# Optimization experiments

Measured on AMD Instinct MI355X. Metric: run time of the kernel, lower is better.

## Reference

```python
import jax, jax.numpy as jnp
import numpy as np

NUM_HEADS = 32
NUM_KV_HEADS = 8
HEAD_DIM = 128
HIDDEN = 4096
THETA = 10000.0


def apply_rotary_emb(x, theta=THETA):
    # x: (B, S, H, D). Torch code converts to complex with real = first half
    # of last dim, imag = second half (rotate-half convention).
    B, S, H, D = x.shape
    half = D // 2
    freqs = 1.0 / theta ** (jnp.arange(0, D, 2, dtype=jnp.float32) / D)  # (half,)
    t = jnp.arange(S, dtype=jnp.float32)
    ang = jnp.outer(t, freqs)  # (S, half)
    cos = jnp.cos(ang)[None, :, None, :]  # (1,S,1,half)
    sin = jnp.sin(ang)[None, :, None, :]
    x1, x2 = x[..., :half], x[..., half:]
    out = jnp.concatenate([x1 * cos - x2 * sin, x1 * sin + x2 * cos], axis=-1)
    return out.astype(x.dtype)


def setup_inputs() -> dict:
    key = jax.random.key(0)
    k1, k2, k3 = jax.random.split(key, 3)
    B, S = 1, 2048
    qkv_out = (NUM_HEADS + 2 * NUM_KV_HEADS) * HEAD_DIM  # 6144
    hidden_states = jax.random.normal(k1, (B, S, HIDDEN), dtype=jnp.float32)
    w_qkv = jax.random.normal(k2, (qkv_out, HIDDEN), dtype=jnp.float32) * 0.02
    w_o = jax.random.normal(k3, (HIDDEN, NUM_HEADS * HEAD_DIM), dtype=jnp.float32) * 0.02
    return {"hidden_states": hidden_states, "w_qkv": w_qkv, "w_o": w_o}


def reference(hidden_states, w_qkv, w_o):
    B, S, _ = hidden_states.shape
    q_size = NUM_HEADS * HEAD_DIM
    kv_size = NUM_KV_HEADS * HEAD_DIM
    n_rep = NUM_HEADS // NUM_KV_HEADS

    qkv = hidden_states @ w_qkv.T  # (B,S,6144)
    xq = qkv[..., :q_size].reshape(B, S, NUM_HEADS, HEAD_DIM)
    xk = qkv[..., q_size:q_size + kv_size].reshape(B, S, NUM_KV_HEADS, HEAD_DIM)
    xv = qkv[..., q_size + kv_size:].reshape(B, S, NUM_KV_HEADS, HEAD_DIM)

    xq = apply_rotary_emb(xq)
    xk = apply_rotary_emb(xk)

    # repeat_interleave KV heads to match query heads
    xk = jnp.repeat(xk, n_rep, axis=2)
    xv = jnp.repeat(xv, n_rep, axis=2)

    q = xq.transpose(0, 2, 1, 3)  # (B,H,S,D)
    k = xk.transpose(0, 2, 1, 3)
    v = xv.transpose(0, 2, 1, 3)

    scale = 1.0 / np.sqrt(HEAD_DIM).astype(np.float32)
    scores = jnp.einsum('bhqd,bhkd->bhqk', q, k) * scale
    causal = jnp.tril(jnp.ones((S, S), dtype=bool))
    scores = jnp.where(causal[None, None], scores, jnp.float32(-jnp.inf))
    attn = jax.nn.softmax(scores, axis=-1)  # dropout=0 (eval)
    out = jnp.einsum('bhqk,bhkd->bhqd', attn, v)
    out = out.transpose(0, 2, 1, 3).reshape(B, S, NUM_HEADS * HEAD_DIM)
    return out @ w_o.T
```

## Files before the change

kernel.cpp:

```cpp
#include <hip/hip_runtime.h>
#include <cstdint>

#define S_LEN 2048
#define HID   4096
#define NHQ   32
#define NKV   8
#define HD    128
#define QKV_N 6144

typedef float  f32x4 __attribute__((ext_vector_type(4)));
typedef short  s16x8 __attribute__((ext_vector_type(8)));
typedef unsigned short ushort_t;

typedef __attribute__((address_space(3))) void       lds_void;
typedef const __attribute__((address_space(1))) void gbl_void;

__device__ __forceinline__ void gload_lds16(const void* g, void* l) {
  __builtin_amdgcn_global_load_lds((gbl_void*)g, (lds_void*)l, 16, 0, 0);
}

__device__ __forceinline__ short f2bf_bits(float f) {
  union { __bf16 b; short s; } u;
  u.b = (__bf16)f;
  return u.s;
}
__device__ __forceinline__ float bf2f(unsigned short u) {
  union { unsigned int i; float f; } x;
  x.i = ((unsigned int)u) << 16;
  return x.f;
}

__device__ __forceinline__ void cvt8(const float* src, ushort_t* dst, int j) {
  const f32x4* s = (const f32x4*)src;
  f32x4 a = s[j * 2], b = s[j * 2 + 1];
  s16x8 r;
  r[0] = f2bf_bits(a[0]); r[1] = f2bf_bits(a[1]); r[2] = f2bf_bits(a[2]); r[3] = f2bf_bits(a[3]);
  r[4] = f2bf_bits(b[0]); r[5] = f2bf_bits(b[1]); r[6] = f2bf_bits(b[2]); r[7] = f2bf_bits(b[3]);
  *((s16x8*)dst + j) = r;
}

__global__ __launch_bounds__(256)
void cvt_hw(const float* __restrict__ h, const float* __restrict__ wq,
            ushort_t* __restrict__ hb, ushort_t* __restrict__ wqb) {
  int i = blockIdx.x * 256 + threadIdx.x;
  if (i < 1048576) cvt8(h, hb, i);
  else             cvt8(wq, wqb, i - 1048576);
}

template <int N> __device__ __forceinline__ void wait_vm() {
  if constexpr (N == 6)      asm volatile("s_waitcnt vmcnt(6)" ::: "memory");
  else if constexpr (N == 4) asm volatile("s_waitcnt vmcnt(4)" ::: "memory");
  else                       asm volatile("s_waitcnt vmcnt(0)" ::: "memory");
}

template <bool OUTF32>
__global__ __launch_bounds__(512, 2)
void gemm8p(const ushort_t* __restrict__ Ag, const ushort_t* __restrict__ Bg,
            void* __restrict__ Cp, int M, int N, int K) {
  __shared__ __align__(16) ushort_t As[2][2][256 * 32];
  __shared__ __align__(16) ushort_t Bs[2][2][256 * 32];

  const int t = threadIdx.x;
  const int w = t >> 6, l = t & 63;
  const int n16 = l & 15, quad = l >> 4;
  const int wm = w >> 2, wn = w & 3;
  const int sw16 = (quad ^ (n16 & 3)) * 16;
  const int m0 = blockIdx.x * 256, n0 = blockIdx.y * 256;

  const int srow = t >> 2;
  const int schunk = (t & 3) ^ (srow & 3);
  const ushort_t* Abase = Ag + (size_t)(m0 + srow) * K + schunk * 8;
  const ushort_t* Bbase = Bg + (size_t)(n0 + srow) * K + schunk * 8;
  char* AsB = (char*)&As[0][0][0];
  char* BsB = (char*)&Bs[0][0][0];
  const size_t hstep = (size_t)128 * K;

  auto stageA = [&](int b, int h, int tile) {
    const ushort_t* g = Abase + (size_t)h * hstep + tile * 64;
    gload_lds16(g,      AsB + b * 32768 + h * 8192 + t * 16);
    gload_lds16(g + 32, AsB + b * 32768 + 16384 + h * 8192 + t * 16);
  };
  auto stageB = [&](int b, int h, int tile) {
    const ushort_t* g = Bbase + (size_t)h * hstep + tile * 64;
    gload_lds16(g,      BsB + b * 32768 + h * 8192 + t * 16);
    gload_lds16(g + 32, BsB + b * 32768 + 16384 + h * 8192 + t * 16);
  };

  const int aRowBase = wm * 64 + n16;
  const int bRowBase = wn * 32 + n16;
  const char* AsR = (const char*)AsB;
  const char* BsR = (const char*)BsB;

  f32x4 acc[8][4] = {};
  s16x8 af[4][2];

#define PHASE(b, qm, qn, STAGE, WZ) do {                                            \
    if ((qn) == 0) {                                                                \
      _Pragma("unroll")                                                             \
      for (int mf = 0; mf < 4; mf++)                                                \
        _Pragma("unroll")                                                           \
        for (int ks = 0; ks < 2; ks++)                                              \
          af[mf][ks] = *(const s16x8*)(AsR + (b) * 32768 + ks * 16384 +             \
                        ((qm) * 128 + mf * 16 + aRowBase) * 64 + sw16);             \
    }                                                                               \
    s16x8 bf[2][2];                                                                 \
    _Pragma("unroll")                                                               \
    for (int nf = 0; nf < 2; nf++)                                                  \
      _Pragma("unroll")                                                             \
      for (int ks = 0; ks < 2; ks++)                                                \
        bf[nf][ks] = *(const s16x8*)(BsR + (b) * 32768 + ks * 16384 +               \
                      ((qn) * 128 + nf * 16 + bRowBase) * 64 + sw16);               \
    __builtin_amdgcn_s_setprio(1);                                                  \
    _Pragma("unroll")                                                               \
    for (int ks = 0; ks < 2; ks++)                                                  \
      _Pragma("unroll")                                                             \
      for (int mf = 0; mf < 4; mf++)                                                \
        _Pragma("unroll")                                                           \
        for (int nf = 0; nf < 2; nf++)                                              \
          acc[(qm) * 4 + mf][(qn) * 2 + nf] = __builtin_amdgcn_mfma_f32_16x16x32_bf16( \
              af[mf][ks], bf[nf][ks], acc[(qm) * 4 + mf][(qn) * 2 + nf], 0, 0, 0);  \
    __builtin_amdgcn_s_setprio(0);                                                  \
    STAGE;                                                                          \
    if (WZ) wait_vm<0>(); else wait_vm<6>();                                        \
    asm volatile("" ::: "memory");                                                  \
    __builtin_amdgcn_s_barrier();                                                   \
    asm volatile("" ::: "memory");                                                  \
  } while (0)

  const int NT = K >> 6;
  const int NI = NT >> 1;

  stageA(0, 0, 0); stageA(0, 1, 0); stageB(0, 0, 0); stageB(0, 1, 0);
  stageA(1, 0, 1); stageB(1, 0, 1);
  wait_vm<4>();
  asm volatile("" ::: "memory");
  __builtin_amdgcn_s_barrier();
  asm volatile("" ::: "memory");

  for (int i = 0; i < NI - 1; i++) {
    const int tp1 = 2 * i + 1, tp2 = 2 * i + 2, tp3 = 2 * i + 3;
    PHASE(0, 0, 0, stageA(1, 1, tp1), 0);
    PHASE(0, 0, 1, stageB(1, 1, tp1), 0);
    PHASE(0, 1, 0, stageA(0, 0, tp2), 0);
    PHASE(0, 1, 1, stageB(0, 0, tp2), 0);
    PHASE(1, 0, 0, stageA(0, 1, tp2), 0);
    PHASE(1, 0, 1, stageB(0, 1, tp2), 0);
    PHASE(1, 1, 0, stageA(1, 0, tp3), 0);
    PHASE(1, 1, 1, stageB(1, 0, tp3), 0);
  }
  PHASE(0, 0, 0, stageA(1, 1, NT - 1), 0);
  PHASE(0, 0, 1, stageB(1, 1, NT - 1), 0);
  PHASE(0, 1, 0, ((void)0), 0);
  PHASE(0, 1, 1, ((void)0), 1);
  PHASE(1, 0, 0, ((void)0), 1);
  PHASE(1, 0, 1, ((void)0), 1);
  PHASE(1, 1, 0, ((void)0), 1);
  PHASE(1, 1, 1, ((void)0), 1);
#undef PHASE

#pragma unroll
  for (int a = 0; a < 8; a++)
#pragma unroll
    for (int bq = 0; bq < 4; bq++)
#pragma unroll
      for (int r = 0; r < 4; r++) {
        int row = m0 + (a >> 2) * 128 + wm * 64 + (a & 3) * 16 + quad * 4 + r;
        int col = n0 + (bq >> 1) * 128 + wn * 32 + (bq & 1) * 16 + n16;
        float v = acc[a][bq][r];
        if constexpr (OUTF32) ((float*)Cp)[(size_t)row * N + col] = v;
        else ((ushort_t*)Cp)[(size_t)row * N + col] = (ushort_t)f2bf_bits(v);
      }
}

__global__ __launch_bounds__(256)
void rope_vt_cvtwo(const ushort_t* __restrict__ qkv, ushort_t* __restrict__ Q,
                   ushort_t* __restrict__ Kc, ushort_t* __restrict__ Vt,
                   const float* __restrict__ wo, ushort_t* __restrict__ wob) {
  __shared__ __align__(16) ushort_t tile[64][72];
  const int b = blockIdx.x;
  const int t = threadIdx.x;
  if (b < 2048) {
    const int s = b;
    const float LN1E4_64 = 0.14391156831212787f;
    for (int item = t; item < (NHQ + NKV) * 64; item += 256) {
      int head = item >> 6, i = item & 63;
      float f = expf(-(float)i * LN1E4_64);
      float ang = (float)s * f;
      float sn, cs;
      sincosf(ang, &sn, &cs);
      if (head < NHQ) {
        const ushort_t* src = qkv + (size_t)s * QKV_N + head * HD;
        float x1 = bf2f(src[i]), x2 = bf2f(src[64 + i]);
        const float sc = 0.08838834764831845f;
        ushort_t* dst = Q + ((size_t)head * S_LEN + s) * HD;
        dst[i]      = (ushort_t)f2bf_bits((x1 * cs - x2 * sn) * sc);
        dst[64 + i] = (ushort_t)f2bf_bits((x1 * sn + x2 * cs) * sc);
      } else {
        int kv = head - NHQ;
        const ushort_t* src = qkv + (size_t)s * QKV_N + 4096 + kv * HD;
        float x1 = bf2f(src[i]), x2 = bf2f(src[64 + i]);
        ushort_t* dst = Kc + ((size_t)kv * S_LEN + s) * HD;
        dst[i]      = (ushort_t)f2bf_bits(x1 * cs - x2 * sn);
        dst[64 + i] = (ushort_t)f2bf_bits(x1 * sn + x2 * cs);
      }
    }
  } else if (b < 2560) {
    const int bb = b - 2048;
    const int s0 = (bb & 31) * 64;
    const int by = bb >> 5;
    const int kv = by >> 1;
    const int d0 = (by & 1) * 64;
    {
      int r = t >> 2, c = (t & 3) * 16;
      const ushort_t* src = qkv + (size_t)(s0 + r) * QKV_N + 5120 + kv * HD + d0 + c;
      *(s16x8*)&tile[r][c]     = *(const s16x8*)src;
      *(s16x8*)&tile[r][c + 8] = *(const s16x8*)(src + 8);
    }
    __syncthreads();
    {
      int d = t >> 2, sseg = (t & 3) * 16;
      ushort_t* dst = Vt + ((size_t)kv * HD + d0 + d) * S_LEN + s0 + sseg;
      s16x8 o1, o2;
#pragma unroll
      for (int i = 0; i < 8; i++) { o1[i] = tile[sseg + i][d]; o2[i] = tile[sseg + 8 + i][d]; }
      *(s16x8*)dst = o1;
      *(s16x8*)(dst + 8) = o2;
    }
  } else {
    int j = (b - 2560) * 256 + t;
    cvt8(wo, wob, j);
  }
}

__global__ __launch_bounds__(256)
void attn_kernel(const ushort_t* __restrict__ Q, const ushort_t* __restrict__ Kc,
                 const ushort_t* __restrict__ Vt, ushort_t* __restrict__ Out) {
  __shared__ __align__(16) ushort_t Ks[2][64 * 128];
  __shared__ __align__(16) ushort_t Vs[2][128 * 64];
  __shared__ __align__(16) ushort_t Pl[4][16 * 72];
  const int bx = blockIdx.x;
  const int h = blockIdx.y;
  const int t = threadIdx.x, w = t >> 6, l = t & 63;
  const int n16 = l & 15, quad = l >> 4;
  const int kv = h >> 2;
  const ushort_t* Qh = Q  + (size_t)h  * S_LEN * HD;
  const ushort_t* Kh = Kc + (size_t)kv * S_LEN * HD;
  const ushort_t* Vh = Vt + (size_t)kv * HD * S_LEN;

  const int qtA = bx, qtB = 31 - bx;
  const int q0A = qtA * 64 + w * 16, q0B = qtB * 64 + w * 16;
  const int tripsA = qtA + 1;
  const int TOTAL = 33;

  s16x8 qfA[4], qfB[4];
#pragma unroll
  for (int ks = 0; ks < 4; ks++) {
    qfA[ks] = *(const s16x8*)(Qh + (size_t)(q0A + n16) * HD + ks * 32 + quad * 8);
    qfB[ks] = *(const s16x8*)(Qh + (size_t)(q0B + n16) * HD + ks * 32 + quad * 8);
  }

  s16x8 ones;
  {
    short v = (n16 == 0) ? (short)0x3F80 : (short)0;
#pragma unroll
    for (int j = 0; j < 8; j++) ones[j] = v;
  }

  f32x4 o[9] = {};
  float mrun[4] = {-1e30f, -1e30f, -1e30f, -1e30f};

  ushort_t* P = Pl[w];

  auto stage = [&](int k0, int buf) {
#pragma unroll
    for (int c = 0; c < 4; c++) {
      int idx = (c * 4 + w) * 64 + l;
      int row = idx >> 4, sc = idx & 15;
      int dseg = sc ^ (row & 15);
      gload_lds16(Kh + (size_t)(k0 + row) * HD + dseg * 8,
                  (char*)&Ks[buf][0] + (c * 4 + w) * 1024);
    }
#pragma unroll
    for (int c = 0; c < 4; c++) {
      int idx = (c * 4 + w) * 64 + l;
      int row = idx >> 3, sc = idx & 7;
      int ks2 = sc ^ (row & 7);
      gload_lds16(Vh + (size_t)row * S_LEN + k0 + ks2 * 8,
                  (char*)&Vs[buf][0] + (c * 4 + w) * 1024);
    }
  };

  stage(0, 0);

  for (int i = 0; i < TOTAL; i++) {
    const bool isA = (i < tripsA);
    const int kt = isA ? i : i - tripsA;
    const int q0 = isA ? q0A : q0B;
    const int k0 = kt * 64;
    const int buf = i & 1;

    __syncthreads();

    if (i + 1 < TOTAL) {
      const bool nA = (i + 1 < tripsA);
      const int nkt = nA ? (i + 1) : (i + 1 - tripsA);
      stage(nkt * 64, buf ^ 1);
    }

    const ushort_t* KsB = &Ks[buf][0];
    const ushort_t* VsB = &Vs[buf][0];

    f32x4 sacc[4] = {};
#pragma unroll
    for (int ks = 0; ks < 4; ks++) {
      s16x8 qf = isA ? qfA[ks] : qfB[ks];
#pragma unroll
      for (int nt = 0; nt < 4; nt++) {
        int row = nt * 16 + n16;
        s16x8 kf = *(const s16x8*)(KsB + row * 128 + ((ks * 4 + quad) ^ (row & 15)) * 8);
        sacc[nt] = __builtin_amdgcn_mfma_f32_16x16x32_bf16(qf, kf, sacc[nt], 0, 0, 0);
      }
    }

    if (k0 + 63 > q0) {
#pragma unroll
      for (int nt = 0; nt < 4; nt++)
#pragma unroll
        for (int r = 0; r < 4; r++) {
          int qrow = q0 + quad * 4 + r;
          int key  = k0 + nt * 16 + n16;
          if (key > qrow) sacc[nt][r] = -1e30f;
        }
    }

#pragma unroll
    for (int r = 0; r < 4; r++) {
      float tmx = fmaxf(fmaxf(sacc[0][r], sacc[1][r]), fmaxf(sacc[2][r], sacc[3][r]));
#pragma unroll
      for (int d = 1; d < 16; d <<= 1) tmx = fmaxf(tmx, __shfl_xor(tmx, d));
      float nm = fmaxf(mrun[r], tmx);
      float alpha = __expf(mrun[r] - nm);
      mrun[r] = nm;
#pragma unroll
      for (int nt = 0; nt < 4; nt++) sacc[nt][r] = __expf(sacc[nt][r] - nm);
#pragma unroll
      for (int nt2 = 0; nt2 < 9; nt2++) o[nt2][r] *= alpha;
    }

#pragma unroll
    for (int nt = 0; nt < 4; nt++)
#pragma unroll
      for (int r = 0; r < 4; r++)
        P[(quad * 4 + r) * 72 + nt * 16 + n16] = (ushort_t)f2bf_bits(sacc[nt][r]);
    asm volatile("s_waitcnt lgkmcnt(0)" ::: "memory");
    s16x8 pa[2];
#pragma unroll
    for (int kseg = 0; kseg < 2; kseg++)
      pa[kseg] = *(const s16x8*)(P + n16 * 72 + kseg * 32 + quad * 8);

#pragma unroll
    for (int kseg = 0; kseg < 2; kseg++) {
#pragma unroll
      for (int ntd = 0; ntd < 8; ntd++) {
        int row = ntd * 16 + n16;
        s16x8 vf = *(const s16x8*)(VsB + row * 64 + ((kseg * 4 + quad) ^ (row & 7)) * 8);
        o[ntd] = __builtin_amdgcn_mfma_f32_16x16x32_bf16(pa[kseg], vf, o[ntd], 0, 0, 0);
      }
      o[8] = __builtin_amdgcn_mfma_f32_16x16x32_bf16(pa[kseg], ones, o[8], 0, 0, 0);
    }

    if (i == tripsA - 1) {
#pragma unroll
      for (int r = 0; r < 4; r++) {
        float lsum = __shfl(o[8][r], l & 48);
        float inv = 1.0f / lsum;
        int qrow = q0A + quad * 4 + r;
#pragma unroll
        for (int ntd = 0; ntd < 8; ntd++)
          Out[(size_t)qrow * HID + h * HD + ntd * 16 + n16] = (ushort_t)f2bf_bits(o[ntd][r] * inv);
      }
#pragma unroll
      for (int nt2 = 0; nt2 < 9; nt2++) o[nt2] = (f32x4){0.f, 0.f, 0.f, 0.f};
#pragma unroll
      for (int r = 0; r < 4; r++) mrun[r] = -1e30f;
    }
  }

#pragma unroll
  for (int r = 0; r < 4; r++) {
    float lsum = __shfl(o[8][r], l & 48);
    float inv = 1.0f / lsum;
    int qrow = q0B + quad * 4 + r;
#pragma unroll
    for (int ntd = 0; ntd < 8; ntd++)
      Out[(size_t)qrow * HID + h * HD + ntd * 16 + n16] = (ushort_t)f2bf_bits(o[ntd][r] * inv);
  }
}

extern "C" void kernel_launch(void* const* d_in, const int* in_sizes, int n_in,
                              void* d_out, int out_size, void* d_ws, size_t ws_size,
                              hipStream_t stream) {
  const float* hidden = (const float*)d_in[0];
  const float* w_qkv  = (const float*)d_in[1];
  const float* w_o    = (const float*)d_in[2];
  float* out = (float*)d_out;
  char* ws = (char*)d_ws;

  ushort_t* hidden_bf = (ushort_t*)ws;
  ushort_t* Qb        = (ushort_t*)ws;
  ushort_t* wqkv_bf   = (ushort_t*)(ws + 16777216);
  ushort_t* wo_bf     = (ushort_t*)(ws + 16777216);
  ushort_t* qkv       = (ushort_t*)(ws + 67108864);
  ushort_t* attn_out  = (ushort_t*)(ws + 67108864);
  ushort_t* Kb        = (ushort_t*)(ws + 92274688);
  ushort_t* Vtb       = (ushort_t*)(ws + 96468992);

  cvt_hw<<<dim3(16384), 256, 0, stream>>>(hidden, w_qkv, hidden_bf, wqkv_bf);
  gemm8p<false><<<dim3(8, 24), 512, 0, stream>>>(hidden_bf, wqkv_bf, (void*)qkv, 2048, 6144, 4096);
  rope_vt_cvtwo<<<dim3(10752), 256, 0, stream>>>(qkv, Qb, Kb, Vtb, w_o, wo_bf);
  attn_kernel<<<dim3(16, 32), 256, 0, stream>>>(Qb, Kb, Vtb, attn_out);
  gemm8p<true><<<dim3(8, 16), 512, 0, stream>>>(attn_out, wo_bf, (void*)out, 2048, 4096, 4096);
}
```

Measured before the change: 560.2 us.

## Restructure GEMM main loop into serpentine phases with B-fragment register reuse

Reworks the 256x256 bf16 GEMM inner loop so each phase issues its LDS reads and next global-to-LDS stage before a barrier and then runs the MFMAs. The quadrant order now snakes (00,01,11,10) so A or B fragments are reused across consecutive phases, using two B fragment register sets. This cuts LDS read traffic. Vmem waits happen only every fourth phase instead of every phase, and the prologue prefetch order changes to match. The cost is more registers, and the barrier and lgkm wait placement adds risk of stalls or races if the staging order is off.

```diff
diff --git a/kernel.cpp b/kernel.cpp
--- a/kernel.cpp
+++ b/kernel.cpp
@@ -88,75 +88,82 @@
 
   const int aRowBase = wm * 64 + n16;
   const int bRowBase = wn * 32 + n16;
-  const char* AsR = (const char*)AsB;
-  const char* BsR = (const char*)BsB;
 
   f32x4 acc[8][4] = {};
-  s16x8 af[4][2];
-
-#define PHASE(b, qm, qn, STAGE, WZ) do {                                            \
-    if ((qn) == 0) {                                                                \
-      _Pragma("unroll")                                                             \
-      for (int mf = 0; mf < 4; mf++)                                                \
-        _Pragma("unroll")                                                           \
-        for (int ks = 0; ks < 2; ks++)                                              \
-          af[mf][ks] = *(const s16x8*)(AsR + (b) * 32768 + ks * 16384 +             \
-                        ((qm) * 128 + mf * 16 + aRowBase) * 64 + sw16);             \
-    }                                                                               \
-    s16x8 bf[2][2];                                                                 \
-    _Pragma("unroll")                                                               \
-    for (int nf = 0; nf < 2; nf++)                                                  \
-      _Pragma("unroll")                                                             \
-      for (int ks = 0; ks < 2; ks++)                                                \
-        bf[nf][ks] = *(const s16x8*)(BsR + (b) * 32768 + ks * 16384 +               \
-                      ((qn) * 128 + nf * 16 + bRowBase) * 64 + sw16);               \
-    __builtin_amdgcn_s_setprio(1);                                                  \
-    _Pragma("unroll")                                                               \
-    for (int ks = 0; ks < 2; ks++)                                                  \
-      _Pragma("unroll")                                                             \
-      for (int mf = 0; mf < 4; mf++)                                                \
-        _Pragma("unroll")                                                           \
-        for (int nf = 0; nf < 2; nf++)                                              \
-          acc[(qm) * 4 + mf][(qn) * 2 + nf] = __builtin_amdgcn_mfma_f32_16x16x32_bf16( \
-              af[mf][ks], bf[nf][ks], acc[(qm) * 4 + mf][(qn) * 2 + nf], 0, 0, 0);  \
-    __builtin_amdgcn_s_setprio(0);                                                  \
-    STAGE;                                                                          \
-    if (WZ) wait_vm<0>(); else wait_vm<6>();                                        \
-    asm volatile("" ::: "memory");                                                  \
-    __builtin_amdgcn_s_barrier();                                                   \
-    asm volatile("" ::: "memory");                                                  \
+  s16x8 af[4][2], bf0[2][2], bf1[2][2];
+
+#define RD_A(b, qm) do {                                                        \
+    _Pragma("unroll")                                                           \
+    for (int mf = 0; mf < 4; mf++)                                              \
+      _Pragma("unroll")                                                         \
+      for (int ks = 0; ks < 2; ks++)                                            \
+        af[mf][ks] = *(const s16x8*)(AsB + (b) * 32768 + ks * 16384 +           \
+                      ((qm) * 128 + mf * 16 + aRowBase) * 64 + sw16);           \
+  } while (0)
+
+#define RD_B(b, qn, dst) do {                                                   \
+    _Pragma("unroll")                                                           \
+    for (int nf = 0; nf < 2; nf++)                                              \
+      _Pragma("unroll")                                                         \
+      for (int ks = 0; ks < 2; ks++)                                            \
+        dst[nf][ks] = *(const s16x8*)(BsB + (b) * 32768 + ks * 16384 +          \
+                      ((qn) * 128 + nf * 16 + bRowBase) * 64 + sw16);           \
+  } while (0)
+
+#define PHASE(RDS, STG, qm, qn, BFX, VMW) do {                                  \
+    RDS;                                                                        \
+    STG;                                                                        \
+    __builtin_amdgcn_s_barrier();                                               \
+    asm volatile("s_waitcnt lgkmcnt(0)" ::: "memory");                          \
+    __builtin_amdgcn_sched_barrier(0);                                          \
+    __builtin_amdgcn_s_setprio(1);                                              \
+    _Pragma("unroll")                                                           \
+    for (int ks = 0; ks < 2; ks++)                                              \
+      _Pragma("unroll")                                                         \
+      for (int mf = 0; mf < 4; mf++)                                            \
+        _Pragma("unroll")                                                       \
+        for (int nf = 0; nf < 2; nf++)                                          \
+          acc[(qm) * 4 + mf][(qn) * 2 + nf] =                                   \
+            __builtin_amdgcn_mfma_f32_16x16x32_bf16(af[mf][ks], BFX[nf][ks],    \
+                acc[(qm) * 4 + mf][(qn) * 2 + nf], 0, 0, 0);                    \
+    __builtin_amdgcn_s_setprio(0);                                              \
+    VMW;                                                                        \
+    __builtin_amdgcn_s_barrier();                                               \
+    asm volatile("" ::: "memory");                                              \
   } while (0)
 
   const int NT = K >> 6;
   const int NI = NT >> 1;
 
-  stageA(0, 0, 0); stageA(0, 1, 0); stageB(0, 0, 0); stageB(0, 1, 0);
-  stageA(1, 0, 1); stageB(1, 0, 1);
-  wait_vm<4>();
+  stageA(0, 0, 0); stageB(0, 0, 0); stageB(0, 1, 0); stageA(0, 1, 0);
+  stageA(1, 0, 1); stageB(1, 0, 1); stageB(1, 1, 1);
+  wait_vm<6>();
   asm volatile("" ::: "memory");
   __builtin_amdgcn_s_barrier();
   asm volatile("" ::: "memory");
 
   for (int i = 0; i < NI - 1; i++) {
-    const int tp1 = 2 * i + 1, tp2 = 2 * i + 2, tp3 = 2 * i + 3;
-    PHASE(0, 0, 0, stageA(1, 1, tp1), 0);
-    PHASE(0, 0, 1, stageB(1, 1, tp1), 0);
-    PHASE(0, 1, 0, stageA(0, 0, tp2), 0);
-    PHASE(0, 1, 1, stageB(0, 0, tp2), 0);
-    PHASE(1, 0, 0, stageA(0, 1, tp2), 0);
-    PHASE(1, 0, 1, stageB(0, 1, tp2), 0);
-    PHASE(1, 1, 0, stageA(1, 0, tp3), 0);
-    PHASE(1, 1, 1, stageB(1, 0, tp3), 0);
-  }
-  PHASE(0, 0, 0, stageA(1, 1, NT - 1), 0);
-  PHASE(0, 0, 1, stageB(1, 1, NT - 1), 0);
-  PHASE(0, 1, 0, ((void)0), 0);
-  PHASE(0, 1, 1, ((void)0), 1);
-  PHASE(1, 0, 0, ((void)0), 1);
-  PHASE(1, 0, 1, ((void)0), 1);
-  PHASE(1, 1, 0, ((void)0), 1);
-  PHASE(1, 1, 1, ((void)0), 1);
+    const int t1 = 2 * i + 1, t0n = 2 * i + 2, t1n = 2 * i + 3;
+    PHASE(RD_A(0, 0); RD_B(0, 0, bf0), stageA(1, 1, t1),  0, 0, bf0, ((void)0));
+    PHASE(RD_B(0, 1, bf1),             stageA(0, 0, t0n), 0, 1, bf1, ((void)0));
+    PHASE(RD_A(0, 1),                  stageB(0, 0, t0n), 1, 1, bf1, ((void)0));
+    PHASE(((void)0),                   stageB(0, 1, t0n), 1, 0, bf0, wait_vm<6>());
+    PHASE(RD_A(1, 0); RD_B(1, 0, bf0), stageA(0, 1, t0n), 0, 0, bf0, ((void)0));
+    PHASE(RD_B(1, 1, bf1),             stageA(1, 0, t1n), 0, 1, bf1, ((void)0));
+    PHASE(RD_A(1, 1),                  stageB(1, 0, t1n), 1, 1, bf1, ((void)0));
+    PHASE(((void)0),                   stageB(1, 1, t1n), 1, 0, bf0, wait_vm<6>());
+  }
+  PHASE(RD_A(0, 0); RD_B(0, 0, bf0), stageA(1, 1, NT - 1), 0, 0, bf0, ((void)0));
+  PHASE(RD_B(0, 1, bf1),             ((void)0),            0, 1, bf1, ((void)0));
+  PHASE(RD_A(0, 1),                  ((void)0),            1, 1, bf1, ((void)0));
+  PHASE(((void)0),                   ((void)0),            1, 0, bf0, wait_vm<0>());
+  PHASE(RD_A(1, 0); RD_B(1, 0, bf0), ((void)0),            0, 0, bf0, ((void)0));
+  PHASE(RD_B(1, 1, bf1),             ((void)0),            0, 1, bf1, ((void)0));
+  PHASE(RD_A(1, 1),                  ((void)0),            1, 1, bf1, ((void)0));
+  PHASE(((void)0),                   ((void)0),            1, 0, bf0, ((void)0));
 #undef PHASE
+#undef RD_A
+#undef RD_B
 
 #pragma unroll
   for (int a = 0; a < 8; a++)
```

Result: slower. 576.1 us (+2.8%).
